# Kernel tuning notes

Hardware: AMD Instinct MI355X
Metric: run time of the kernel (lower is better)

The kernel has to match this reference:

```python
import jax, jax.numpy as jnp
import numpy as np

B = 262144
G = 21       # number of groups (hardcoded in the torch forward)
GS = 8       # features per group
BASIC = 13   # data[:, :13]
H = 512      # hidden_dim
OUT = 1      # output_size


def setup_inputs() -> dict:
    key = jax.random.key(0)
    k0, k1, k2, k3, k4, k5, k6 = jax.random.split(key, 7)
    data = jax.random.normal(k0, (B, BASIC + G * GS), dtype=jnp.float32)
    # per-group Linear(GS, 1): stacked weights [G, GS] and biases [G]
    gW = jax.random.normal(k1, (G, GS), dtype=jnp.float32) * 0.1
    gb = jax.random.normal(k2, (G,), dtype=jnp.float32) * 0.1
    W1 = jax.random.normal(k3, (BASIC + G, H), dtype=jnp.float32) * 0.1
    b1 = jax.random.normal(k4, (H,), dtype=jnp.float32) * 0.1
    W2 = jax.random.normal(k5, (H, OUT), dtype=jnp.float32) * 0.1
    b2 = jax.random.normal(k6, (OUT,), dtype=jnp.float32) * 0.1
    return {"data": data, "gW": gW, "gb": gb, "W1": W1, "b1": b1, "W2": W2, "b2": b2}


def reference(data, gW, gb, W1, b1, W2, b2):
    # Groups are the contiguous, exclusive column slices 13:181 -> [B, G, GS].
    grouped = data[:, BASIC:].reshape(data.shape[0], G, GS)
    # 21 tiny Linear(GS,1)+Sigmoid ops, fused into one batched contraction.
    gout = jax.nn.sigmoid(jnp.einsum("bgd,gd->bg", grouped, gW) + gb)  # [B, G]
    mixed = jnp.concatenate([data[:, :BASIC], gout], axis=1)           # [B, 13+21]
    h = jax.nn.relu(mixed @ W1 + b1)                                   # [B, H]
    return jax.nn.sigmoid(h @ W2 + b2)                                 # [B, OUT]
```

## Files before the change

kernel.cpp:

```cpp
#include <hip/hip_runtime.h>
#include <hip/hip_bf16.h>


#define B_ROWS 262144
#define DFEAT  181
#define BASICF 13
#define NG     21
#define MIXF   34
#define HID    512
#define NT     1024
#define TILE   256
#define MSTRIDE 40
#define ROWS_PER_BLOCK 512
#define NTILES (ROWS_PER_BLOCK / TILE)
#define NBLK   (B_ROWS / ROWS_PER_BLOCK)

typedef __attribute__((ext_vector_type(8))) short short8;
typedef __attribute__((ext_vector_type(4))) float float4_t;

__device__ __forceinline__ short f2bf(float f) {
    union { float f; unsigned u; } v; v.f = f;
    unsigned r = (v.u + 0x7FFFu + ((v.u >> 16) & 1u)) >> 16;
    return (short)r;
}
__device__ __forceinline__ float sigm(float x) { return 1.0f / (1.0f + __expf(-x)); }

__device__ __forceinline__ float4_t load4u(const float* p) {
    float4_t v;
    __builtin_memcpy(&v, p, 16);
    return v;
}

__device__ __forceinline__ void build_rows(
    const float* __restrict__ data, int row0_global, int wave, int lane,
    float4_t gwv, float gbv, short* __restrict__ mixed, float* __restrict__ mtail)
{
    #pragma unroll 4
    for (int rr = 0; rr < 16; ++rr) {
        const int row = wave * 16 + rr;
        const float* dr = data + (size_t)(row0_global + row) * DFEAT;
        if (lane < 42) {
            float4_t x = load4u(dr + BASICF + lane * 4);
            float p = fmaf(x[0], gwv[0],
                      fmaf(x[1], gwv[1],
                      fmaf(x[2], gwv[2], x[3] * gwv[3])));
            p += __shfl_xor(p, 1, 64);
            if ((lane & 1) == 0) {
                int g = lane >> 1;
                float v = sigm(p + gbv);
                if (g < 19) mixed[row * MSTRIDE + BASICF + g] = f2bf(v);
                else        mtail[row * 2 + (g - 19)] = v;
            }
        } else if (lane >= 43 && lane < 56) {
            int c = lane - 43;
            mixed[row * MSTRIDE + c] = f2bf(dr[c]);
        }
    }
}

__global__ __launch_bounds__(NT) void fused_mfma_kernel(
    const float* __restrict__ data, const float* __restrict__ gW,
    const float* __restrict__ gb, const float* __restrict__ W1,
    const float* __restrict__ b1, const float* __restrict__ W2,
    const float* __restrict__ b2, float* __restrict__ out)
{
    __shared__ __align__(16) short   W1f[32 * 64 * 8];
    __shared__ __align__(16) float4_t wbt[HID];
    __shared__ __align__(16) short   mixed[TILE * MSTRIDE];
    __shared__ __align__(8)  float   mtail[TILE * 2];

    const int tid = threadIdx.x;

    for (int idx = tid; idx < 32 * HID; idx += NT) {
        int k = idx >> 9, c = idx & 511;
        int t = c >> 4, ci = c & 15;
        int l = ((k >> 3) << 4) + ci;
        int j = k & 7;
        W1f[(t * 64 + l) * 8 + j] = f2bf(W1[k * HID + c]);
    }
    if (tid < HID) {
        int c = tid;
        wbt[c] = (float4_t){ b1[c], W2[c], W1[32 * HID + c], W1[33 * HID + c] };
    }

    const int wave = tid >> 6;
    const int lane = tid & 63;
    const int lg   = lane >> 4;
    const int li   = lane & 15;

    float4_t gwv = {0.f, 0.f, 0.f, 0.f};
    float gbv = 0.f;
    if (lane < 42) {
        gwv = ((const float4_t*)gW)[lane];
        gbv = gb[lane >> 1];
    }
    const float b2v = b2[0];
    const int blk_row0 = blockIdx.x * ROWS_PER_BLOCK;
    __syncthreads();

    build_rows(data, blk_row0, wave, lane, gwv, gbv, mixed, mtail);
    __syncthreads();

    for (int tile = 0; tile < NTILES; ++tile) {
        const int trow0 = blk_row0 + tile * TILE;

        short8 a0 = *(const short8*)&mixed[(wave * 16 + li) * MSTRIDE + lg * 8];
        float2 mt[4];
        #pragma unroll
        for (int j = 0; j < 4; ++j)
            mt[j] = *(const float2*)&mtail[(wave * 16 + lg * 4 + j) * 2];
        __syncthreads();

        if (tile + 1 < NTILES)
            build_rows(data, trow0 + TILE, wave, lane, gwv, gbv, mixed, mtail);

        float4_t acc = {0.f, 0.f, 0.f, 0.f};
        for (int t = 0; t < 32; ++t) {
            short8 bf = *(const short8*)&W1f[(t * 64 + lane) * 8];
            float4_t c4 = {0.f, 0.f, 0.f, 0.f};
            c4 = __builtin_amdgcn_mfma_f32_16x16x32_bf16(a0, bf, c4, 0, 0, 0);
            int c = t * 16 + li;
            float4_t wv = wbt[c];
            #pragma unroll
            for (int j = 0; j < 4; ++j) {
                float h = c4[j] + wv.x;
                h = fmaf(mt[j].x, wv.z, h);
                h = fmaf(mt[j].y, wv.w, h);
                h = fmaxf(h, 0.f);
                acc[j] = fmaf(h, wv.y, acc[j]);
            }
        }
        #pragma unroll
        for (int m = 1; m < 16; m <<= 1) {
            #pragma unroll
            for (int j = 0; j < 4; ++j) acc[j] += __shfl_xor(acc[j], m, 64);
        }
        if (li == 0) {
            #pragma unroll
            for (int j = 0; j < 4; ++j)
                out[trow0 + wave * 16 + lg * 4 + j] = sigm(acc[j] + b2v);
        }
        __syncthreads();
    }
}

extern "C" void kernel_launch(void* const* d_in, const int* in_sizes, int n_in,
                              void* d_out, int out_size, void* d_ws, size_t ws_size,
                              hipStream_t stream) {
    (void)in_sizes; (void)n_in; (void)out_size; (void)d_ws; (void)ws_size;
    const float* data = (const float*)d_in[0];
    const float* gW   = (const float*)d_in[1];
    const float* gb   = (const float*)d_in[2];
    const float* W1   = (const float*)d_in[3];
    const float* b1   = (const float*)d_in[4];
    const float* W2   = (const float*)d_in[5];
    const float* b2   = (const float*)d_in[6];
    float* out = (float*)d_out;
    fused_mfma_kernel<<<dim3(NBLK), dim3(NT), 0, stream>>>(data, gW, gb, W1, b1, W2, b2, out);
}
```

Measured before the change: 53.92 us.

## Fold bias and tail features into an extra MFMA, process 512 rows per block

Removes the two-tile software pipeline and instead builds all 512 rows of the block into shared memory at once, so each wave computes two 16-row M tiles. The two tail group features plus a constant 1 are packed into a second bf16 MFMA against the matching W1 rows and b1, which replaces the per-element scalar bias and tail FMAs in the epilogue. Bias, W2 and the tail weights are stored as packed bf16, which lowers their precision. The overlap of building the next tile with compute is lost, and the larger mixed buffer increases LDS use.

After: 54.40 us. Within noise of the previous version (+0.9%).

```diff
diff --git a/kernel.cpp b/kernel.cpp
--- a/kernel.cpp
+++ b/kernel.cpp
@@ -6,13 +6,10 @@
 #define DFEAT  181
 #define BASICF 13
 #define NG     21
-#define MIXF   34
 #define HID    512
 #define NT     1024
-#define TILE   256
 #define MSTRIDE 40
 #define ROWS_PER_BLOCK 512
-#define NTILES (ROWS_PER_BLOCK / TILE)
 #define NBLK   (B_ROWS / ROWS_PER_BLOCK)
 
 typedef __attribute__((ext_vector_type(8))) short short8;
@@ -23,6 +20,10 @@
     unsigned r = (v.u + 0x7FFFu + ((v.u >> 16) & 1u)) >> 16;
     return (short)r;
 }
+__device__ __forceinline__ float bfhi2f(unsigned u) {
+    union { unsigned u; float f; } v; v.u = u;
+    return v.f;
+}
 __device__ __forceinline__ float sigm(float x) { return 1.0f / (1.0f + __expf(-x)); }
 
 __device__ __forceinline__ float4_t load4u(const float* p) {
@@ -31,45 +32,21 @@
     return v;
 }
 
-__device__ __forceinline__ void build_rows(
-    const float* __restrict__ data, int row0_global, int wave, int lane,
-    float4_t gwv, float gbv, short* __restrict__ mixed, float* __restrict__ mtail)
-{
-    #pragma unroll 4
-    for (int rr = 0; rr < 16; ++rr) {
-        const int row = wave * 16 + rr;
-        const float* dr = data + (size_t)(row0_global + row) * DFEAT;
-        if (lane < 42) {
-            float4_t x = load4u(dr + BASICF + lane * 4);
-            float p = fmaf(x[0], gwv[0],
-                      fmaf(x[1], gwv[1],
-                      fmaf(x[2], gwv[2], x[3] * gwv[3])));
-            p += __shfl_xor(p, 1, 64);
-            if ((lane & 1) == 0) {
-                int g = lane >> 1;
-                float v = sigm(p + gbv);
-                if (g < 19) mixed[row * MSTRIDE + BASICF + g] = f2bf(v);
-                else        mtail[row * 2 + (g - 19)] = v;
-            }
-        } else if (lane >= 43 && lane < 56) {
-            int c = lane - 43;
-            mixed[row * MSTRIDE + c] = f2bf(dr[c]);
-        }
-    }
-}
-
 __global__ __launch_bounds__(NT) void fused_mfma_kernel(
     const float* __restrict__ data, const float* __restrict__ gW,
     const float* __restrict__ gb, const float* __restrict__ W1,
     const float* __restrict__ b1, const float* __restrict__ W2,
     const float* __restrict__ b2, float* __restrict__ out)
 {
-    __shared__ __align__(16) short   W1f[32 * 64 * 8];
-    __shared__ __align__(16) float4_t wbt[HID];
-    __shared__ __align__(16) short   mixed[TILE * MSTRIDE];
-    __shared__ __align__(8)  float   mtail[TILE * 2];
+    __shared__ __align__(16) short W1f[32 * 64 * 8];
+    __shared__ __align__(8)  int   wbt2[HID * 2];
+    __shared__ __align__(16) short mixed[ROWS_PER_BLOCK * MSTRIDE];
 
-    const int tid = threadIdx.x;
+    const int tid  = threadIdx.x;
+    const int wave = tid >> 6;
+    const int lane = tid & 63;
+    const int lg   = lane >> 4;
+    const int li   = lane & 15;
 
     for (int idx = tid; idx < 32 * HID; idx += NT) {
         int k = idx >> 9, c = idx & 511;
@@ -80,13 +57,13 @@
     }
     if (tid < HID) {
         int c = tid;
-        wbt[c] = (float4_t){ b1[c], W2[c], W1[32 * HID + c], W1[33 * HID + c] };
+        unsigned pb  = (unsigned short)f2bf(b1[c]);
+        unsigned pw2 = (unsigned short)f2bf(W2[c]);
+        unsigned pa  = (unsigned short)f2bf(W1[32 * HID + c]);
+        unsigned pbb = (unsigned short)f2bf(W1[33 * HID + c]);
+        wbt2[c * 2 + 0] = (int)(pb | (pw2 << 16));
+        wbt2[c * 2 + 1] = (int)(pa | (pbb << 16));
     }
-
-    const int wave = tid >> 6;
-    const int lane = tid & 63;
-    const int lg   = lane >> 4;
-    const int li   = lane & 15;
 
     float4_t gwv = {0.f, 0.f, 0.f, 0.f};
     float gbv = 0.f;
@@ -96,51 +73,80 @@
     }
     const float b2v = b2[0];
     const int blk_row0 = blockIdx.x * ROWS_PER_BLOCK;
+
+    #pragma unroll 4
+    for (int rr = 0; rr < 32; ++rr) {
+        const int row = wave * 32 + rr;
+        const float* dr = data + (size_t)(blk_row0 + row) * DFEAT;
+        if (lane < 42) {
+            float4_t x = load4u(dr + BASICF + lane * 4);
+            float p = fmaf(x[0], gwv[0],
+                      fmaf(x[1], gwv[1],
+                      fmaf(x[2], gwv[2], x[3] * gwv[3])));
+            p += __shfl_xor(p, 1, 64);
+            if ((lane & 1) == 0) {
+                int g = lane >> 1;
+                float v = sigm(p + gbv);
+                mixed[row * MSTRIDE + BASICF + g] = f2bf(v);
+            }
+        } else if (lane >= 43 && lane < 56) {
+            int c = lane - 43;
+            mixed[row * MSTRIDE + c] = f2bf(dr[c]);
+        }
+    }
     __syncthreads();
 
-    build_rows(data, blk_row0, wave, lane, gwv, gbv, mixed, mtail);
-    __syncthreads();
+    const int r0 = wave * 32;
+    short8 a_lo = *(const short8*)&mixed[(r0 + li) * MSTRIDE + lg * 8];
+    short8 a_hi = *(const short8*)&mixed[(r0 + 16 + li) * MSTRIDE + lg * 8];
+    short8 ab_lo, ab_hi;
+    {
+        int mt_lo = *(const int*)&mixed[(r0 + li) * MSTRIDE + 32];
+        int mt_hi = *(const int*)&mixed[(r0 + 16 + li) * MSTRIDE + 32];
+        union { int i[4]; short8 s; } ua;
+        ua.i[0] = (lg == 0) ? mt_lo : 0;
+        ua.i[1] = (lg == 0) ? 0x00003F80 : 0;
+        ua.i[2] = 0; ua.i[3] = 0;
+        ab_lo = ua.s;
+        ua.i[0] = (lg == 0) ? mt_hi : 0;
+        ab_hi = ua.s;
+    }
 
-    for (int tile = 0; tile < NTILES; ++tile) {
-        const int trow0 = blk_row0 + tile * TILE;
-
-        short8 a0 = *(const short8*)&mixed[(wave * 16 + li) * MSTRIDE + lg * 8];
-        float2 mt[4];
+    float4_t acc_lo = {0.f, 0.f, 0.f, 0.f};
+    float4_t acc_hi = {0.f, 0.f, 0.f, 0.f};
+    const float4_t z4 = {0.f, 0.f, 0.f, 0.f};
+    for (int t = 0; t < 32; ++t) {
+        short8 bf = *(const short8*)&W1f[(t * 64 + lane) * 8];
+        int2 wv = ((const int2*)wbt2)[t * 16 + li];
+        union { int i[4]; short8 s; } ub;
+        ub.i[0] = (lg == 0) ? wv.y : 0;
+        ub.i[1] = (lg == 0) ? (wv.x & 0xffff) : 0;
+        ub.i[2] = 0; ub.i[3] = 0;
+        float4_t c_lo = __builtin_amdgcn_mfma_f32_16x16x32_bf16(ab_lo, ub.s, z4, 0, 0, 0);
+        float4_t c_hi = __builtin_amdgcn_mfma_f32_16x16x32_bf16(ab_hi, ub.s, z4, 0, 0, 0);
+        c_lo = __builtin_amdgcn_mfma_f32_16x16x32_bf16(a_lo, bf, c_lo, 0, 0, 0);
+        c_hi = __builtin_amdgcn_mfma_f32_16x16x32_bf16(a_hi, bf, c_hi, 0, 0, 0);
+        float w2f = bfhi2f((unsigned)wv.x & 0xffff0000u);
         #pragma unroll
-        for (int j = 0; j < 4; ++j)
-            mt[j] = *(const float2*)&mtail[(wave * 16 + lg * 4 + j) * 2];
-        __syncthreads();
-
-        if (tile + 1 < NTILES)
-            build_rows(data, trow0 + TILE, wave, lane, gwv, gbv, mixed, mtail);
-
-        float4_t acc = {0.f, 0.f, 0.f, 0.f};
-        for (int t = 0; t < 32; ++t) {
-            short8 bf = *(const short8*)&W1f[(t * 64 + lane) * 8];
-            float4_t c4 = {0.f, 0.f, 0.f, 0.f};
-            c4 = __builtin_amdgcn_mfma_f32_16x16x32_bf16(a0, bf, c4, 0, 0, 0);
-            int c = t * 16 + li;
-            float4_t wv = wbt[c];
-            #pragma unroll
-            for (int j = 0; j < 4; ++j) {
-                float h = c4[j] + wv.x;
-                h = fmaf(mt[j].x, wv.z, h);
-                h = fmaf(mt[j].y, wv.w, h);
-                h = fmaxf(h, 0.f);
-                acc[j] = fmaf(h, wv.y, acc[j]);
-            }
+        for (int j = 0; j < 4; ++j) {
+            acc_lo[j] = fmaf(fmaxf(c_lo[j], 0.f), w2f, acc_lo[j]);
+            acc_hi[j] = fmaf(fmaxf(c_hi[j], 0.f), w2f, acc_hi[j]);
         }
+    }
+    #pragma unroll
+    for (int m = 1; m < 16; m <<= 1) {
         #pragma unroll
-        for (int m = 1; m < 16; m <<= 1) {
-            #pragma unroll
-            for (int j = 0; j < 4; ++j) acc[j] += __shfl_xor(acc[j], m, 64);
+        for (int j = 0; j < 4; ++j) {
+            acc_lo[j] += __shfl_xor(acc_lo[j], m, 64);
+            acc_hi[j] += __shfl_xor(acc_hi[j], m, 64);
         }
-        if (li == 0) {
-            #pragma unroll
-            for (int j = 0; j < 4; ++j)
-                out[trow0 + wave * 16 + lg * 4 + j] = sigm(acc[j] + b2v);
+    }
+    if (li == 0) {
+        #pragma unroll
+        for (int j = 0; j < 4; ++j) {
+            out[blk_row0 + r0 + lg * 4 + j]      = sigm(acc_lo[j] + b2v);
+            out[blk_row0 + r0 + 16 + lg * 4 + j] = sigm(acc_hi[j] + b2v);
         }
-        __syncthreads();
     }
 }
 
```
